# Performance work log

Hardware: AMD Instinct MI355X
Metric: run time of the kernel (lower is better)

## Reference

```python
import jax, jax.numpy as jnp
import numpy as np

B = 1024      # Monte-Carlo samples (batch)
NX, NY = 8, 8 # lattice size
I = 3         # local Hilbert dim (hole, down, up)
H = 256       # hidden_dim
N_TARGET = 48 # target particle number
SZ = 0        # target magnetization sector


def setup_inputs() -> dict:
    key = jax.random.key(0)
    ks = jax.random.split(key, 8)
    f = jnp.float32
    samples = jax.random.randint(ks[0], (B, NX, NY), 0, 3)
    s_in = 1.0 / np.sqrt(2 * H)
    W1 = jax.random.normal(ks[1], (2 * I, 2 * H, H), f) * s_in
    W2 = jax.random.normal(ks[2], (2 * I, 2 * H, H), f) * s_in
    Wmerge = jax.random.normal(ks[3], (2 * H, H), f) * s_in
    b1 = jnp.full((H,), 0.01, f)
    b2 = jnp.full((H,), 0.01, f)
    s_l = 1.0 / np.sqrt(H)
    Wl1 = jax.random.normal(ks[4], (H, I), f) * s_l
    bl1 = jnp.zeros((I,), f)
    Wl2 = jax.random.normal(ks[5], (H, I), f) * s_l
    bl2 = jnp.zeros((I,), f)
    return {"samples": samples, "W1": W1, "b1": b1, "W2": W2, "b2": b2,
            "Wmerge": Wmerge, "Wl1": Wl1, "bl1": bl1, "Wl2": Wl2, "bl2": bl2}


def _gru_cell(sx, sy, hx, hy, W1, b1, W2, b2, Wmerge):
    # sx,sy: [B,I] one-hot neighbor inputs; hx,hy: [B,H] neighbor hiddens
    st = jnp.concatenate([hx, hy], axis=1)   # [B, 2H]
    inp = jnp.concatenate([sx, sy], axis=1)  # [B, 2I]
    # torch: einsum('ijk,lj->ikl', W, st) then einsum('li,ikl->lk', inp, .)
    pre1 = jnp.einsum('li,ijk,lj->lk', inp, W1, st)
    h_tilde = jnp.tanh(pre1 + b1)
    pre2 = jnp.einsum('li,ijk,lj->lk', inp, W2, st)
    u = jax.nn.sigmoid(pre2 + b2)
    return u * h_tilde + (1.0 - u) * (st @ Wmerge)


def _forward(samples, W1, b1, W2, b2, Wmerge, Wl1, bl1, Wl2, bl2):
    f = W1.dtype
    oh = jax.nn.one_hot(samples, I, dtype=f)  # [B,NX,NY,I]
    z_h = jnp.zeros((B, H), f)
    z_s = jnp.zeros((B, I), f)
    hid = {}
    bl_up = (N_TARGET + 2 * SZ) // 2
    bl_dn = (N_TARGET - 2 * SZ) // 2
    bl_hole = NX * NY - N_TARGET
    n_up = jnp.zeros((B,), f)
    n_dn = jnp.zeros((B,), f)
    log_a = jnp.zeros((B,), f)
    log_p = jnp.zeros((B,), f)
    k = 0  # number of already-sampled sites (static per step)
    for ny in range(NY):
        # snake (zig-zag) ordering over the 2D lattice
        xs = range(NX) if ny % 2 == 0 else range(NX - 1, -1, -1)
        dx = -1 if ny % 2 == 0 else 1
        for nx in xs:
            nxn = nx + dx
            sx = oh[:, nxn, ny] if 0 <= nxn < NX else z_s
            hx = hid.get((nxn, ny), z_h)
            sy = oh[:, nx, ny - 1] if ny > 0 else z_s
            hy = hid.get((nx, ny - 1), z_h)
            h = _gru_cell(sx, sy, hx, hy, W1, b1, W2, b2, Wmerge)
            hid[(nx, ny)] = h
            probs = jax.nn.softmax(h @ Wl1 + bl1, axis=1)          # [B,I]
            phase = jnp.pi * jax.nn.soft_sign(h @ Wl2 + bl2)       # [B,I]
            # enforce particle-number / magnetization sectors (heaviside masks)
            m_up = (bl_up - n_up > 0).astype(f)
            m_dn = (bl_dn - n_dn > 0).astype(f)
            m_hole = (bl_hole - (k - n_up - n_dn) > 0).astype(f)
            mask = jnp.stack([m_hole, m_dn, m_up], axis=1)         # [B,I]
            amp = probs * mask
            amp = amp / jnp.maximum(amp.sum(axis=1, keepdims=True), 1e-30)
            s = samples[:, nx, ny]
            sel = jax.nn.one_hot(s, I, dtype=f)
            log_a = log_a + jnp.log(jnp.clip((amp * sel).sum(axis=1), 1e-12))
            log_p = log_p + (phase * sel).sum(axis=1)
            n_up = n_up + (s == 2).astype(f)
            n_dn = n_dn + (s == 1).astype(f)
            k += 1
    return 0.5 * log_a, log_p


def reference(samples, W1, b1, W2, b2, Wmerge, Wl1, bl1, Wl2, bl2):
    return _forward(samples, W1, b1, W2, b2, Wmerge, Wl1, bl1, Wl2, bl2)
```

## Files before the change

kernel.cpp:

```cpp
#include <hip/hip_runtime.h>
#include <hip/hip_bf16.h>
#include <math.h>

#define Bsz 1024
#define Hd  256
#define MAXTILE 40
#define PERM_PER_CELL (MAXTILE*32)
#define WTSTRIDE (768*512)
#define GHALF (Bsz*768)
#define NPART 4

typedef short bf16x8 __attribute__((ext_vector_type(8)));
typedef float f32x4  __attribute__((ext_vector_type(4)));

__global__ __launch_bounds__(256)
void build_wc(const float* __restrict__ W1, const float* __restrict__ W2,
              const float* __restrict__ Wm,
              __hip_bfloat16* __restrict__ Wht, __hip_bfloat16* __restrict__ Wlt)
{
    size_t idx = (size_t)blockIdx.x * 256 + threadIdx.x;
    int k = (int)(idx & 511);
    size_t rem = idx >> 9;
    int col = (int)(rem % 768);
    int c = (int)(rem / 768);
    int a = c >> 2, b = c & 3;
    float v;
    if (col < 256) {
        v = ((a < 3) ? W1[(size_t)a * 512 * 256 + k * 256 + col] : 0.f)
          + ((b < 3) ? W1[(size_t)(3 + b) * 512 * 256 + k * 256 + col] : 0.f);
    } else if (col < 512) {
        int cc = col - 256;
        v = ((a < 3) ? W2[(size_t)a * 512 * 256 + k * 256 + cc] : 0.f)
          + ((b < 3) ? W2[(size_t)(3 + b) * 512 * 256 + k * 256 + cc] : 0.f);
    } else {
        v = Wm[(size_t)k * 256 + (col - 512)];
    }
    __hip_bfloat16 vh = __float2bfloat16(v);
    __hip_bfloat16 vl = __float2bfloat16(v - __bfloat162float(vh));
    Wht[idx] = vh;
    Wlt[idx] = vl;
}

__global__ __launch_bounds__(256)
void bucketize(const int* __restrict__ samples, int* __restrict__ perm,
               int* __restrict__ tiletab)
{
    const int cell = blockIdx.x;
    const int t = threadIdx.x;
    const int ny = cell >> 3, ixs = cell & 7;
    const int nx  = (ny & 1) ? (7 - ixs) : ixs;
    const int dx  = (ny & 1) ? 1 : -1;
    const int nxn = nx + dx;
    const bool hasX = (nxn >= 0) && (nxn < 8);
    const bool hasY = (ny > 0);
    const int sx_off = nxn * 8 + ny;
    const int sy_off = nx * 8 + ny - 1;

    __shared__ int hist[16], cursor[16];
    int* pcell = perm + (size_t)cell * PERM_PER_CELL;
    for (int i = t; i < PERM_PER_CELL; i += 256) pcell[i] = -1;
    if (t < 16) hist[t] = 0;
    __syncthreads();

    int myc[4];
#pragma unroll
    for (int q = 0; q < 4; q++) {
        int l = t * 4 + q;
        int a = hasX ? samples[l * 64 + sx_off] : 3;
        int b = hasY ? samples[l * 64 + sy_off] : 3;
        myc[q] = a * 4 + b;
        atomicAdd(&hist[myc[q]], 1);
    }
    __syncthreads();

    if (t == 0) {
        int tile = 0, row = 0;
        for (int c = 0; c < 16; c++) {
            cursor[c] = row;
            int nt = (hist[c] + 31) >> 5;
            for (int k = 0; k < nt; k++) tiletab[cell * MAXTILE + tile + k] = c;
            tile += nt;
            row  += nt * 32;
        }
        for (; tile < MAXTILE; tile++) tiletab[cell * MAXTILE + tile] = -1;
    }
    __syncthreads();

#pragma unroll
    for (int q = 0; q < 4; q++) {
        int l = t * 4 + q;
        int pos = atomicAdd(&cursor[myc[q]], 1);
        pcell[pos] = l;
    }
}

__global__ __launch_bounds__(256)
void gemm_mfma(const __hip_bfloat16* __restrict__ hxh, const __hip_bfloat16* __restrict__ hxl,
               const __hip_bfloat16* __restrict__ hyh, const __hip_bfloat16* __restrict__ hyl,
               const __hip_bfloat16* __restrict__ Wht, const __hip_bfloat16* __restrict__ Wlt,
               const int* __restrict__ perm, const int* __restrict__ tiletab,
               float* __restrict__ Gp, int cell, int kbeg, int kend)
{
    const int combo = tiletab[cell * MAXTILE + blockIdx.y];
    if (combo < 0) return;
    const int chunk = blockIdx.z;
    const int kbase = chunk << 7;
    const int lo = (kbeg > kbase) ? kbeg : kbase;
    const int hi = (kend < kbase + 128) ? kend : (kbase + 128);
    const int k0 = blockIdx.x * 64;
    const int* pr = perm + (size_t)cell * PERM_PER_CELL + blockIdx.y * 32;
    float* Gout = Gp + (size_t)chunk * GHALF;

    const int t  = threadIdx.x;
    const int w  = t >> 6;
    const int l  = t & 63;
    const int lr = l & 15;
    const int lg = l >> 4;

    __shared__ __align__(16) short Bh[64 * 128];
    __shared__ __align__(16) short Bl[64 * 128];

    f32x4 acc0 = {0.f, 0.f, 0.f, 0.f};
    f32x4 acc1 = {0.f, 0.f, 0.f, 0.f};

    if (lo < hi) {
        const __hip_bfloat16* baseH = Wht + (size_t)combo * WTSTRIDE + kbase;
        const __hip_bfloat16* baseL = Wlt + (size_t)combo * WTSTRIDE + kbase;
        for (int i = t; i < 1024; i += 256) {
            int c  = i >> 4;
            int kq = i & 15;
            int q  = c * 16 + (kq ^ (c & 7));
            ((uint4*)Bh)[q] = *(const uint4*)(baseH + (size_t)(k0 + c) * 512 + kq * 8);
            ((uint4*)Bl)[q] = *(const uint4*)(baseL + (size_t)(k0 + c) * 512 + kq * 8);
        }
        __syncthreads();

        const __hip_bfloat16* Hh = (chunk < 2) ? hxh : hyh;
        const __hip_bfloat16* Hl = (chunk < 2) ? hxl : hyl;
        const int hbase = kbase - ((chunk < 2) ? 0 : 256);
        const int r0 = pr[lr];
        const int r1 = pr[16 + lr];
        const int cB = w * 16 + lr;

#pragma unroll
        for (int ks = 0; ks < 4; ks++) {
            const int koff = hbase + ks * 32 + lg * 8;
            bf16x8 a0h = (r0 >= 0) ? *(const bf16x8*)(Hh + (size_t)r0 * Hd + koff) : (bf16x8)0;
            bf16x8 a0l = (r0 >= 0) ? *(const bf16x8*)(Hl + (size_t)r0 * Hd + koff) : (bf16x8)0;
            bf16x8 a1h = (r1 >= 0) ? *(const bf16x8*)(Hh + (size_t)r1 * Hd + koff) : (bf16x8)0;
            bf16x8 a1l = (r1 >= 0) ? *(const bf16x8*)(Hl + (size_t)r1 * Hd + koff) : (bf16x8)0;

            const int kq = ks * 4 + lg;
            const int q  = cB * 16 + (kq ^ (cB & 7));
            bf16x8 bh = ((const bf16x8*)Bh)[q];
            bf16x8 bl = ((const bf16x8*)Bl)[q];

            acc0 = __builtin_amdgcn_mfma_f32_16x16x32_bf16(a0h, bh, acc0, 0, 0, 0);
            acc0 = __builtin_amdgcn_mfma_f32_16x16x32_bf16(a0h, bl, acc0, 0, 0, 0);
            acc0 = __builtin_amdgcn_mfma_f32_16x16x32_bf16(a0l, bh, acc0, 0, 0, 0);
            acc1 = __builtin_amdgcn_mfma_f32_16x16x32_bf16(a1h, bh, acc1, 0, 0, 0);
            acc1 = __builtin_amdgcn_mfma_f32_16x16x32_bf16(a1h, bl, acc1, 0, 0, 0);
            acc1 = __builtin_amdgcn_mfma_f32_16x16x32_bf16(a1l, bh, acc1, 0, 0, 0);
        }
    }

    const int colA = k0 + w * 16 + lr;
#pragma unroll
    for (int reg = 0; reg < 4; reg++) {
        const int rl = 4 * lg + reg;
        int ra = pr[rl];
        if (ra >= 0) Gout[(size_t)ra * 768 + colA] = acc0[reg];
        int rb = pr[16 + rl];
        if (rb >= 0) Gout[(size_t)rb * 768 + colA] = acc1[reg];
    }
}

__global__ __launch_bounds__(256)
void combine_logprob(const float* __restrict__ Gp, const int* __restrict__ samples,
                     const float* __restrict__ b1, const float* __restrict__ b2,
                     const float* __restrict__ Wl1, const float* __restrict__ bl1,
                     const float* __restrict__ Wl2, const float* __restrict__ bl2,
                     __hip_bfloat16* __restrict__ houth, __hip_bfloat16* __restrict__ houtl,
                     float* __restrict__ acc, float* __restrict__ out,
                     int s_off, int kcell)
{
    const int l = blockIdx.x;
    const int k = threadIdx.x;
    const float* g0 = Gp + (size_t)l * 768;

    float pre1 = b1[k], pre2 = b2[k], mg = 0.f;
#pragma unroll
    for (int z = 0; z < NPART; z++) {
        const float* g = g0 + (size_t)z * GHALF;
        pre1 += g[k];
        pre2 += g[256 + k];
        mg   += g[512 + k];
    }
    float ht = tanhf(pre1);
    float u  = 1.0f / (1.0f + expf(-pre2));
    float h  = u * ht + (1.0f - u) * mg;
    __hip_bfloat16 hh = __float2bfloat16(h);
    __hip_bfloat16 hl = __float2bfloat16(h - __bfloat162float(hh));
    houth[(size_t)l * Hd + k] = hh;
    houtl[(size_t)l * Hd + k] = hl;

    float v[6];
    v[0] = h * Wl1[k * 3 + 0];
    v[1] = h * Wl1[k * 3 + 1];
    v[2] = h * Wl1[k * 3 + 2];
    v[3] = h * Wl2[k * 3 + 0];
    v[4] = h * Wl2[k * 3 + 1];
    v[5] = h * Wl2[k * 3 + 2];
#pragma unroll
    for (int m = 1; m < 64; m <<= 1)
#pragma unroll
        for (int i = 0; i < 6; i++) v[i] += __shfl_xor(v[i], m);

    __shared__ float red[4][6];
    if ((k & 63) == 0) {
#pragma unroll
        for (int i = 0; i < 6; i++) red[k >> 6][i] = v[i];
    }
    __syncthreads();

    if (k == 0) {
        float p1[3], p2[3];
#pragma unroll
        for (int i = 0; i < 3; i++) {
            p1[i] = red[0][i]     + red[1][i]     + red[2][i]     + red[3][i];
            p2[i] = red[0][3 + i] + red[1][3 + i] + red[2][3 + i] + red[3][3 + i];
        }
        float la, lp, nu, nd;
        if (kcell == 0) { la = 0.f; lp = 0.f; nu = 0.f; nd = 0.f; }
        else {
            la = acc[l];           lp = acc[Bsz + l];
            nu = acc[2 * Bsz + l]; nd = acc[3 * Bsz + l];
        }
        float z0 = p1[0] + bl1[0], z1 = p1[1] + bl1[1], z2 = p1[2] + bl1[2];
        float zm = fmaxf(z0, fmaxf(z1, z2));
        float e0 = expf(z0 - zm), e1 = expf(z1 - zm), e2 = expf(z2 - zm);
        float es = e0 + e1 + e2;
        float mh = (16.0f - ((float)kcell - nu - nd) > 0.0f) ? 1.0f : 0.0f;
        float md = (24.0f - nd > 0.0f) ? 1.0f : 0.0f;
        float mu = (24.0f - nu > 0.0f) ? 1.0f : 0.0f;
        float a0 = (e0 / es) * mh, a1 = (e1 / es) * md, a2 = (e2 / es) * mu;
        float asum = fmaxf(a0 + a1 + a2, 1e-30f);
        int sv = samples[l * 64 + s_off];
        float av = ((sv == 0) ? a0 : (sv == 1) ? a1 : a2) / asum;
        float q  = p2[sv] + bl2[sv];
        float ph = 3.14159265358979323846f * (q / (1.0f + fabsf(q)));
        la += logf(fmaxf(av, 1e-12f));
        lp += ph;
        nu += (sv == 2) ? 1.0f : 0.0f;
        nd += (sv == 1) ? 1.0f : 0.0f;
        acc[l] = la; acc[Bsz + l] = lp;
        acc[2 * Bsz + l] = nu; acc[3 * Bsz + l] = nd;
        if (kcell == 63) {
            out[l]       = 0.5f * la;
            out[Bsz + l] = lp;
        }
    }
}

extern "C" void kernel_launch(void* const* d_in, const int* in_sizes, int n_in,
                              void* d_out, int out_size, void* d_ws, size_t ws_size,
                              hipStream_t stream)
{
    const int*   samples = (const int*)  d_in[0];
    const float* W1  = (const float*)d_in[1];
    const float* b1  = (const float*)d_in[2];
    const float* W2  = (const float*)d_in[3];
    const float* b2  = (const float*)d_in[4];
    const float* Wm  = (const float*)d_in[5];
    const float* Wl1 = (const float*)d_in[6];
    const float* bl1 = (const float*)d_in[7];
    const float* Wl2 = (const float*)d_in[8];
    const float* bl2 = (const float*)d_in[9];

    float* ws = (float*)d_ws;
    float* Gp  = ws;
    float* acc = Gp + (size_t)NPART * GHALF;
    __hip_bfloat16* Hh  = (__hip_bfloat16*)(acc + 4 * Bsz);
    __hip_bfloat16* Hl  = Hh + (size_t)8 * Bsz * Hd;
    __hip_bfloat16* Wht = Hl + (size_t)8 * Bsz * Hd;
    __hip_bfloat16* Wlt = Wht + (size_t)16 * WTSTRIDE;
    int* perm    = (int*)(Wlt + (size_t)16 * WTSTRIDE);
    int* tiletab = perm + (size_t)64 * PERM_PER_CELL;
    float* out = (float*)d_out;

    build_wc<<<dim3(16 * 768 * 512 / 256), dim3(256), 0, stream>>>(W1, W2, Wm, Wht, Wlt);
    bucketize<<<dim3(64), dim3(256), 0, stream>>>(samples, perm, tiletab);

    int kcell = 0;
    for (int ny = 0; ny < 8; ny++) {
        const int x0  = (ny % 2 == 0) ? 0 : 7;
        const int dxs = (ny % 2 == 0) ? 1 : -1;
        const int dx  = (ny % 2 == 0) ? -1 : 1;
        for (int ix = 0; ix < 8; ix++) {
            const int nx  = x0 + ix * dxs;
            const int nxn = nx + dx;
            const bool hasX = (nxn >= 0 && nxn < 8);
            const bool hasY = (ny > 0);
            const __hip_bfloat16* hxh = hasX ? (Hh + (size_t)nxn * Bsz * Hd) : nullptr;
            const __hip_bfloat16* hxl = hasX ? (Hl + (size_t)nxn * Bsz * Hd) : nullptr;
            const __hip_bfloat16* hyh = hasY ? (Hh + (size_t)nx  * Bsz * Hd) : nullptr;
            const __hip_bfloat16* hyl = hasY ? (Hl + (size_t)nx  * Bsz * Hd) : nullptr;
            const int kbeg = hasX ? 0   : 256;
            const int kend = hasY ? 512 : 256;

            gemm_mfma<<<dim3(12, MAXTILE, NPART), dim3(256), 0, stream>>>(
                hxh, hxl, hyh, hyl, Wht, Wlt, perm, tiletab, Gp, kcell, kbeg, kend);

            combine_logprob<<<dim3(Bsz), dim3(256), 0, stream>>>(
                Gp, samples, b1, b2, Wl1, bl1, Wl2, bl2,
                Hh + (size_t)nx * Bsz * Hd, Hl + (size_t)nx * Bsz * Hd,
                acc, out, nx * 8 + ny, kcell);
            kcell++;
        }
    }
}
```

Measured before the change: 1.958 ms.

## Replace per-combo bucketed GEMM with dense 13-block GEMM and gather in combine

Drops the sample bucketing by neighbor-input combo. Instead, every sample's hidden state is multiplied against all 13 weight blocks (W1 and W2 slices for each one-hot input, plus Wmerge) in one dense GEMM, and the combine kernel picks the needed blocks using the sample values. This removes the perm/tiletab indirection, the padded partial tiles and the four-way K-split partial buffers, and the new GEMM reuses each A fragment across 7 column fragments per wave. In exchange it does more MFMA work per cell, since all 12 input-dependent blocks are computed rather than only the selected pair.

```diff
diff --git a/kernel.cpp b/kernel.cpp
--- a/kernel.cpp
+++ b/kernel.cpp
@@ -4,197 +4,139 @@
 
 #define Bsz 1024
 #define Hd  256
-#define MAXTILE 40
-#define PERM_PER_CELL (MAXTILE*32)
-#define WTSTRIDE (768*512)
-#define GHALF (Bsz*768)
-#define NPART 4
+#define NCOL 3328
+#define NCOLP 3344
 
 typedef short bf16x8 __attribute__((ext_vector_type(8)));
 typedef float f32x4  __attribute__((ext_vector_type(4)));
 
 __global__ __launch_bounds__(256)
-void build_wc(const float* __restrict__ W1, const float* __restrict__ W2,
-              const float* __restrict__ Wm,
-              __hip_bfloat16* __restrict__ Wht, __hip_bfloat16* __restrict__ Wlt)
+void build_wc13(const float* __restrict__ W1, const float* __restrict__ W2,
+                const float* __restrict__ Wm,
+                __hip_bfloat16* __restrict__ Wht, __hip_bfloat16* __restrict__ Wlt)
 {
     size_t idx = (size_t)blockIdx.x * 256 + threadIdx.x;
-    int k = (int)(idx & 511);
-    size_t rem = idx >> 9;
-    int col = (int)(rem % 768);
-    int c = (int)(rem / 768);
-    int a = c >> 2, b = c & 3;
-    float v;
-    if (col < 256) {
-        v = ((a < 3) ? W1[(size_t)a * 512 * 256 + k * 256 + col] : 0.f)
-          + ((b < 3) ? W1[(size_t)(3 + b) * 512 * 256 + k * 256 + col] : 0.f);
-    } else if (col < 512) {
-        int cc = col - 256;
-        v = ((a < 3) ? W2[(size_t)a * 512 * 256 + k * 256 + cc] : 0.f)
-          + ((b < 3) ? W2[(size_t)(3 + b) * 512 * 256 + k * 256 + cc] : 0.f);
-    } else {
-        v = Wm[(size_t)k * 256 + (col - 512)];
-    }
-    __hip_bfloat16 vh = __float2bfloat16(v);
-    __hip_bfloat16 vl = __float2bfloat16(v - __bfloat162float(vh));
+    int k   = (int)(idx & 511);
+    int col = (int)(idx >> 9);
+    int v   = col >> 8;
+    int cc  = col & 255;
+    float val;
+    if (v < 6)       val = W1[(size_t)v * 512 * 256 + k * 256 + cc];
+    else if (v < 12) val = W2[(size_t)(v - 6) * 512 * 256 + k * 256 + cc];
+    else             val = Wm[(size_t)k * 256 + cc];
+    __hip_bfloat16 vh = __float2bfloat16(val);
+    __hip_bfloat16 vl = __float2bfloat16(val - __bfloat162float(vh));
     Wht[idx] = vh;
     Wlt[idx] = vl;
 }
 
-__global__ __launch_bounds__(256)
-void bucketize(const int* __restrict__ samples, int* __restrict__ perm,
-               int* __restrict__ tiletab)
-{
-    const int cell = blockIdx.x;
-    const int t = threadIdx.x;
-    const int ny = cell >> 3, ixs = cell & 7;
-    const int nx  = (ny & 1) ? (7 - ixs) : ixs;
-    const int dx  = (ny & 1) ? 1 : -1;
-    const int nxn = nx + dx;
-    const bool hasX = (nxn >= 0) && (nxn < 8);
-    const bool hasY = (ny > 0);
-    const int sx_off = nxn * 8 + ny;
-    const int sy_off = nx * 8 + ny - 1;
-
-    __shared__ int hist[16], cursor[16];
-    int* pcell = perm + (size_t)cell * PERM_PER_CELL;
-    for (int i = t; i < PERM_PER_CELL; i += 256) pcell[i] = -1;
-    if (t < 16) hist[t] = 0;
-    __syncthreads();
-
-    int myc[4];
-#pragma unroll
-    for (int q = 0; q < 4; q++) {
-        int l = t * 4 + q;
-        int a = hasX ? samples[l * 64 + sx_off] : 3;
-        int b = hasY ? samples[l * 64 + sy_off] : 3;
-        myc[q] = a * 4 + b;
-        atomicAdd(&hist[myc[q]], 1);
-    }
-    __syncthreads();
-
-    if (t == 0) {
-        int tile = 0, row = 0;
-        for (int c = 0; c < 16; c++) {
-            cursor[c] = row;
-            int nt = (hist[c] + 31) >> 5;
-            for (int k = 0; k < nt; k++) tiletab[cell * MAXTILE + tile + k] = c;
-            tile += nt;
-            row  += nt * 32;
-        }
-        for (; tile < MAXTILE; tile++) tiletab[cell * MAXTILE + tile] = -1;
-    }
-    __syncthreads();
-
-#pragma unroll
-    for (int q = 0; q < 4; q++) {
-        int l = t * 4 + q;
-        int pos = atomicAdd(&cursor[myc[q]], 1);
-        pcell[pos] = l;
-    }
-}
-
-__global__ __launch_bounds__(256)
-void gemm_mfma(const __hip_bfloat16* __restrict__ hxh, const __hip_bfloat16* __restrict__ hxl,
-               const __hip_bfloat16* __restrict__ hyh, const __hip_bfloat16* __restrict__ hyl,
-               const __hip_bfloat16* __restrict__ Wht, const __hip_bfloat16* __restrict__ Wlt,
-               const int* __restrict__ perm, const int* __restrict__ tiletab,
-               float* __restrict__ Gp, int cell, int kbeg, int kend)
-{
-    const int combo = tiletab[cell * MAXTILE + blockIdx.y];
-    if (combo < 0) return;
-    const int chunk = blockIdx.z;
-    const int kbase = chunk << 7;
-    const int lo = (kbeg > kbase) ? kbeg : kbase;
-    const int hi = (kend < kbase + 128) ? kend : (kbase + 128);
-    const int k0 = blockIdx.x * 64;
-    const int* pr = perm + (size_t)cell * PERM_PER_CELL + blockIdx.y * 32;
-    float* Gout = Gp + (size_t)chunk * GHALF;
+__global__ __launch_bounds__(512)
+void gemm13(const __hip_bfloat16* __restrict__ Hxh, const __hip_bfloat16* __restrict__ Hxl,
+            const __hip_bfloat16* __restrict__ Hyh, const __hip_bfloat16* __restrict__ Hyl,
+            const __hip_bfloat16* __restrict__ Wht, const __hip_bfloat16* __restrict__ Wlt,
+            float* __restrict__ Gall, int pbeg, int pend)
+{
+    const int suboff[4] = {0, 7, 14, 20};
+    const int subcnt[4] = {7, 7, 6, 6};
+    const int bid    = blockIdx.x;
+    const int xcd    = bid & 7;
+    const int rowtile= (bid >> 3) & 7;
+    const int colsub = bid >> 6;
+    const int fragbase = xcd * 26 + suboff[colsub];
+    const int nfrag    = subcnt[colsub];
+    const int colbase  = fragbase * 16;
+    const int rowbase  = rowtile * 128;
 
     const int t  = threadIdx.x;
     const int w  = t >> 6;
     const int l  = t & 63;
     const int lr = l & 15;
     const int lg = l >> 4;
-
-    __shared__ __align__(16) short Bh[64 * 128];
-    __shared__ __align__(16) short Bl[64 * 128];
-
-    f32x4 acc0 = {0.f, 0.f, 0.f, 0.f};
-    f32x4 acc1 = {0.f, 0.f, 0.f, 0.f};
-
-    if (lo < hi) {
-        const __hip_bfloat16* baseH = Wht + (size_t)combo * WTSTRIDE + kbase;
-        const __hip_bfloat16* baseL = Wlt + (size_t)combo * WTSTRIDE + kbase;
-        for (int i = t; i < 1024; i += 256) {
-            int c  = i >> 4;
-            int kq = i & 15;
-            int q  = c * 16 + (kq ^ (c & 7));
-            ((uint4*)Bh)[q] = *(const uint4*)(baseH + (size_t)(k0 + c) * 512 + kq * 8);
-            ((uint4*)Bl)[q] = *(const uint4*)(baseL + (size_t)(k0 + c) * 512 + kq * 8);
-        }
+    const int wrow = rowbase + w * 16;
+    const int arow = wrow + lr;
+
+    __shared__ __align__(16) short BhS[112 * 72];
+    __shared__ __align__(16) short BlS[112 * 72];
+
+    f32x4 acc[7];
+#pragma unroll
+    for (int f = 0; f < 7; f++) acc[f] = (f32x4){0.f, 0.f, 0.f, 0.f};
+
+    for (int p = pbeg; p < pend; p++) {
         __syncthreads();
-
-        const __hip_bfloat16* Hh = (chunk < 2) ? hxh : hyh;
-        const __hip_bfloat16* Hl = (chunk < 2) ? hxl : hyl;
-        const int hbase = kbase - ((chunk < 2) ? 0 : 256);
-        const int r0 = pr[lr];
-        const int r1 = pr[16 + lr];
-        const int cB = w * 16 + lr;
-
-#pragma unroll
-        for (int ks = 0; ks < 4; ks++) {
-            const int koff = hbase + ks * 32 + lg * 8;
-            bf16x8 a0h = (r0 >= 0) ? *(const bf16x8*)(Hh + (size_t)r0 * Hd + koff) : (bf16x8)0;
-            bf16x8 a0l = (r0 >= 0) ? *(const bf16x8*)(Hl + (size_t)r0 * Hd + koff) : (bf16x8)0;
-            bf16x8 a1h = (r1 >= 0) ? *(const bf16x8*)(Hh + (size_t)r1 * Hd + koff) : (bf16x8)0;
-            bf16x8 a1l = (r1 >= 0) ? *(const bf16x8*)(Hl + (size_t)r1 * Hd + koff) : (bf16x8)0;
-
-            const int kq = ks * 4 + lg;
-            const int q  = cB * 16 + (kq ^ (cB & 7));
-            bf16x8 bh = ((const bf16x8*)Bh)[q];
-            bf16x8 bl = ((const bf16x8*)Bl)[q];
-
-            acc0 = __builtin_amdgcn_mfma_f32_16x16x32_bf16(a0h, bh, acc0, 0, 0, 0);
-            acc0 = __builtin_amdgcn_mfma_f32_16x16x32_bf16(a0h, bl, acc0, 0, 0, 0);
-            acc0 = __builtin_amdgcn_mfma_f32_16x16x32_bf16(a0l, bh, acc0, 0, 0, 0);
-            acc1 = __builtin_amdgcn_mfma_f32_16x16x32_bf16(a1h, bh, acc1, 0, 0, 0);
-            acc1 = __builtin_amdgcn_mfma_f32_16x16x32_bf16(a1h, bl, acc1, 0, 0, 0);
-            acc1 = __builtin_amdgcn_mfma_f32_16x16x32_bf16(a1l, bh, acc1, 0, 0, 0);
-        }
-    }
-
-    const int colA = k0 + w * 16 + lr;
-#pragma unroll
-    for (int reg = 0; reg < 4; reg++) {
-        const int rl = 4 * lg + reg;
-        int ra = pr[rl];
-        if (ra >= 0) Gout[(size_t)ra * 768 + colA] = acc0[reg];
-        int rb = pr[16 + rl];
-        if (rb >= 0) Gout[(size_t)rb * 768 + colA] = acc1[reg];
+        for (int i = t; i < 896; i += 512) {
+            int c = i >> 3, q = i & 7;
+            size_t src = (size_t)(colbase + c) * 512 + p * 64 + q * 8;
+            *(uint4*)&BhS[c * 72 + q * 8] = *(const uint4*)&Wht[src];
+            *(uint4*)&BlS[c * 72 + q * 8] = *(const uint4*)&Wlt[src];
+        }
+        __syncthreads();
+
+#pragma unroll
+        for (int ks2 = 0; ks2 < 2; ks2++) {
+            const int ks = p * 2 + ks2;
+            const __hip_bfloat16* Ah_ = (ks < 8) ? Hxh : Hyh;
+            const __hip_bfloat16* Al_ = (ks < 8) ? Hxl : Hyl;
+            const int koff = ((ks & 7) * 32) + lg * 8;
+            bf16x8 ah = *(const bf16x8*)(Ah_ + (size_t)arow * Hd + koff);
+            bf16x8 al = *(const bf16x8*)(Al_ + (size_t)arow * Hd + koff);
+
+            const int kloc = ks2 * 32 + lg * 8;
+            bf16x8 bh[7], bl[7];
+#pragma unroll
+            for (int f = 0; f < 7; f++) {
+                bh[f] = *(const bf16x8*)&BhS[(f * 16 + lr) * 72 + kloc];
+                bl[f] = *(const bf16x8*)&BlS[(f * 16 + lr) * 72 + kloc];
+            }
+#pragma unroll
+            for (int f = 0; f < 7; f++)
+                acc[f] = __builtin_amdgcn_mfma_f32_16x16x32_bf16(ah, bh[f], acc[f], 0, 0, 0);
+#pragma unroll
+            for (int f = 0; f < 7; f++)
+                acc[f] = __builtin_amdgcn_mfma_f32_16x16x32_bf16(ah, bl[f], acc[f], 0, 0, 0);
+#pragma unroll
+            for (int f = 0; f < 7; f++)
+                acc[f] = __builtin_amdgcn_mfma_f32_16x16x32_bf16(al, bh[f], acc[f], 0, 0, 0);
+        }
+    }
+
+#pragma unroll
+    for (int f = 0; f < 7; f++) {
+        if (f < nfrag) {
+            const int col = colbase + f * 16 + lr;
+#pragma unroll
+            for (int reg = 0; reg < 4; reg++) {
+                const int row = wrow + 4 * lg + reg;
+                Gall[(size_t)row * NCOL + col] = acc[f][reg];
+            }
+        }
     }
 }
 
 __global__ __launch_bounds__(256)
-void combine_logprob(const float* __restrict__ Gp, const int* __restrict__ samples,
-                     const float* __restrict__ b1, const float* __restrict__ b2,
-                     const float* __restrict__ Wl1, const float* __restrict__ bl1,
-                     const float* __restrict__ Wl2, const float* __restrict__ bl2,
-                     __hip_bfloat16* __restrict__ houth, __hip_bfloat16* __restrict__ houtl,
-                     float* __restrict__ acc, float* __restrict__ out,
-                     int s_off, int kcell)
+void combine13(const float* __restrict__ Gall, const int* __restrict__ samples,
+               const float* __restrict__ b1, const float* __restrict__ b2,
+               const float* __restrict__ Wl1, const float* __restrict__ bl1,
+               const float* __restrict__ Wl2, const float* __restrict__ bl2,
+               __hip_bfloat16* __restrict__ houth, __hip_bfloat16* __restrict__ houtl,
+               float* __restrict__ acc, float* __restrict__ out,
+               int sx_off, int sy_off, int s_off, int kcell)
 {
     const int l = blockIdx.x;
     const int k = threadIdx.x;
-    const float* g0 = Gp + (size_t)l * 768;
-
-    float pre1 = b1[k], pre2 = b2[k], mg = 0.f;
-#pragma unroll
-    for (int z = 0; z < NPART; z++) {
-        const float* g = g0 + (size_t)z * GHALF;
-        pre1 += g[k];
-        pre2 += g[256 + k];
-        mg   += g[512 + k];
+    const float* g = Gall + (size_t)l * NCOL;
+
+    float pre1 = b1[k], pre2 = b2[k];
+    float mg = g[12 * 256 + k];
+    if (sx_off >= 0) {
+        int ix = samples[l * 64 + sx_off];
+        pre1 += g[ix * 256 + k];
+        pre2 += g[(6 + ix) * 256 + k];
+    }
+    if (sy_off >= 0) {
+        int iy = samples[l * 64 + sy_off];
+        pre1 += g[(3 + iy) * 256 + k];
+        pre2 += g[(9 + iy) * 256 + k];
     }
     float ht = tanhf(pre1);
     float u  = 1.0f / (1.0f + expf(-pre2));
@@ -278,18 +220,15 @@
     const float* bl2 = (const float*)d_in[9];
 
     float* ws = (float*)d_ws;
-    float* Gp  = ws;
-    float* acc = Gp + (size_t)NPART * GHALF;
+    float* Gall = ws;
+    float* acc  = Gall + (size_t)Bsz * NCOL;
     __hip_bfloat16* Hh  = (__hip_bfloat16*)(acc + 4 * Bsz);
     __hip_bfloat16* Hl  = Hh + (size_t)8 * Bsz * Hd;
     __hip_bfloat16* Wht = Hl + (size_t)8 * Bsz * Hd;
-    __hip_bfloat16* Wlt = Wht + (size_t)16 * WTSTRIDE;
-    int* perm    = (int*)(Wlt + (size_t)16 * WTSTRIDE);
-    int* tiletab = perm + (size_t)64 * PERM_PER_CELL;
+    __hip_bfloat16* Wlt = Wht + (size_t)NCOLP * 512;
     float* out = (float*)d_out;
 
-    build_wc<<<dim3(16 * 768 * 512 / 256), dim3(256), 0, stream>>>(W1, W2, Wm, Wht, Wlt);
-    bucketize<<<dim3(64), dim3(256), 0, stream>>>(samples, perm, tiletab);
+    build_wc13<<<dim3(NCOL * 512 / 256), dim3(256), 0, stream>>>(W1, W2, Wm, Wht, Wlt);
 
     int kcell = 0;
     for (int ny = 0; ny < 8; ny++) {
@@ -301,20 +240,21 @@
             const int nxn = nx + dx;
             const bool hasX = (nxn >= 0 && nxn < 8);
             const bool hasY = (ny > 0);
-            const __hip_bfloat16* hxh = hasX ? (Hh + (size_t)nxn * Bsz * Hd) : nullptr;
-            const __hip_bfloat16* hxl = hasX ? (Hl + (size_t)nxn * Bsz * Hd) : nullptr;
-            const __hip_bfloat16* hyh = hasY ? (Hh + (size_t)nx  * Bsz * Hd) : nullptr;
-            const __hip_bfloat16* hyl = hasY ? (Hl + (size_t)nx  * Bsz * Hd) : nullptr;
-            const int kbeg = hasX ? 0   : 256;
-            const int kend = hasY ? 512 : 256;
-
-            gemm_mfma<<<dim3(12, MAXTILE, NPART), dim3(256), 0, stream>>>(
-                hxh, hxl, hyh, hyl, Wht, Wlt, perm, tiletab, Gp, kcell, kbeg, kend);
-
-            combine_logprob<<<dim3(Bsz), dim3(256), 0, stream>>>(
-                Gp, samples, b1, b2, Wl1, bl1, Wl2, bl2,
-                Hh + (size_t)nx * Bsz * Hd, Hl + (size_t)nx * Bsz * Hd,
-                acc, out, nx * 8 + ny, kcell);
+            const int pbeg = hasX ? 0 : 4;
+            const int pend = hasY ? 8 : 4;
+            const size_t slotX = (size_t)(hasX ? nxn : 0) * Bsz * Hd;
+            const size_t slotY = (size_t)nx * Bsz * Hd;
+
+            gemm13<<<dim3(256), dim3(512), 0, stream>>>(
+                Hh + slotX, Hl + slotX, Hh + slotY, Hl + slotY,
+                Wht, Wlt, Gall, pbeg, pend);
+
+            const int sx_off = hasX ? (nxn * 8 + ny)       : -1;
+            const int sy_off = hasY ? (nx  * 8 + (ny - 1)) : -1;
+            combine13<<<dim3(Bsz), dim3(256), 0, stream>>>(
+                Gall, samples, b1, b2, Wl1, bl1, Wl2, bl2,
+                Hh + slotY, Hl + slotY, acc, out,
+                sx_off, sy_off, nx * 8 + ny, kcell);
             kcell++;
         }
     }
```

Result: faster. 1.753 ms (-10.5%).
